# Kernel tuning notes

Measured on AMD Instinct MI355X. Metric: run time of the kernel, lower is better.

Reference implementation:

```python
import jax, jax.numpy as jnp
import numpy as np

N_NODES = 100000
N_EDGES = 1600000
IN_C, HID_C, OUT_C = 128, 64, 32


def setup_inputs() -> dict:
    key = jax.random.key(0)
    k1, k2, k3, k4 = jax.random.split(key, 4)
    x = jax.random.normal(k1, (N_NODES, IN_C), dtype=jnp.float32)
    edge_index = jax.random.randint(k2, (2, N_EDGES), 0, N_NODES, dtype=jnp.int64)
    # glorot-style init for GCN linear weights
    W1 = jax.random.normal(k3, (IN_C, HID_C), dtype=jnp.float32) * (2.0 / (IN_C + HID_C)) ** 0.5
    b1 = jnp.zeros((HID_C,), dtype=jnp.float32)
    W2 = jax.random.normal(k4, (HID_C, OUT_C), dtype=jnp.float32) * (2.0 / (HID_C + OUT_C)) ** 0.5
    b2 = jnp.zeros((OUT_C,), dtype=jnp.float32)
    return {"x": x, "edge_index": edge_index, "W1": W1, "b1": b1, "W2": W2, "b2": b2}


def _gcn_conv(h, row, col, norm, n, b):
    # gather transformed source features, scale by symmetric norm, scatter-add to targets
    msg = h[row] * norm[:, None]            # [E+N, C]
    return jax.ops.segment_sum(msg, col, num_segments=n) + b


def reference(x, edge_index, W1, b1, W2, b2):
    n = x.shape[0]
    loops = jnp.arange(n, dtype=edge_index.dtype)
    row = jnp.concatenate([edge_index[0], loops])   # sources (with self-loops)
    col = jnp.concatenate([edge_index[1], loops])   # targets
    deg = jax.ops.segment_sum(jnp.ones_like(col, dtype=x.dtype), col, num_segments=n)
    dinv = jnp.where(deg > 0, jax.lax.rsqrt(deg), 0.0)
    norm = dinv[row] * dinv[col]                    # D^{-1/2} A_hat D^{-1/2}
    h = jax.nn.relu(_gcn_conv(x @ W1, row, col, norm, n, b1))
    out = _gcn_conv(h @ W2, row, col, norm, n, b2)
    return out
```

## Files before the change

### kernel.cpp

```cpp
#include <hip/hip_runtime.h>

#define IN_C 128
#define HID_C 64
#define OUT_C 32
#define NBLK 512
#define NBUCK 512
#define CAP 5120

__device__ __forceinline__ void f4add(float4& a, const float4 b) {
  a.x += b.x; a.y += b.y; a.z += b.z; a.w += b.w;
}


__global__ void __launch_bounds__(256) scatter_reserve_kernel(
    const int* __restrict__ row, const int* __restrict__ col,
    int* __restrict__ gcur, int* __restrict__ ebuf, int e, int epb) {
  __shared__ int hist[NBUCK];
  __shared__ int cur[NBUCK];
  int t = threadIdx.x, b = blockIdx.x;
  for (int i = t; i < NBUCK; i += 256) hist[i] = 0;
  __syncthreads();
  int s = b * epb, en = min(e, s + epb);
  for (int i = s + t; i < en; i += 256) atomicAdd(&hist[col[i] >> 8], 1);
  __syncthreads();
  for (int i = t; i < NBUCK; i += 256) {
    int h = hist[i];
    int base = h ? atomicAdd(&gcur[i], h) : 0;
    cur[i] = CAP * i + base;
  }
  __syncthreads();
  for (int i = s + t; i < en; i += 256) {
    int c = col[i], r = row[i];
    int bk = c >> 8;
    int p = atomicAdd(&cur[bk], 1);
    if (p < CAP * bk + CAP) ebuf[p] = r | ((c & 255) << 17);
  }
}

__global__ void __launch_bounds__(512) bstart_scan_kernel(const int* __restrict__ gcur,
                                                          int* __restrict__ bstart) {
  __shared__ int s[NBUCK];
  int t = threadIdx.x;
  int v = min(gcur[t], CAP);
  s[t] = v;
  __syncthreads();
  for (int d = 1; d < NBUCK; d <<= 1) {
    int a = (t >= d) ? s[t - d] : 0;
    __syncthreads();
    s[t] += a;
    __syncthreads();
  }
  bstart[t] = s[t] - v;
}

__global__ void __launch_bounds__(256) csr_kernel(const int* __restrict__ ebuf,
                                                  const int* __restrict__ gcur,
                                                  const int* __restrict__ bstart,
                                                  int* __restrict__ offS, int* __restrict__ offE,
                                                  int* __restrict__ srt, float* __restrict__ dinv,
                                                  int n) {
  __shared__ int cnt[256];
  __shared__ int base[256];
  int t = threadIdx.x, b = blockIdx.x;
  int es = b * CAP;
  int ec = min(gcur[b], CAP);
  cnt[t] = 0;
  __syncthreads();
  for (int i = t; i < ec; i += 256) atomicAdd(&cnt[(ebuf[es + i] >> 17) & 255], 1);
  __syncthreads();
  int v = cnt[t];
  base[t] = v;
  __syncthreads();
  for (int d = 1; d < 256; d <<= 1) {
    int a = (t >= d) ? base[t - d] : 0;
    __syncthreads();
    base[t] += a;
    __syncthreads();
  }
  int gstart = bstart[b] + base[t] - v;
  int node = b * 256 + t;
  if (node < n) {
    offS[node] = gstart;
    offE[node] = gstart + v;
    dinv[node] = rsqrtf((float)(v + 1));
  }
  base[t] = gstart;
  __syncthreads();
  for (int i = t; i < ec; i += 256) {
    int pv = ebuf[es + i];
    int pos = atomicAdd(&base[(pv >> 17) & 255], 1);
    srt[pos] = pv & 0x1FFFF;
  }
}


__global__ void gemm1_kernel(const float* __restrict__ x, const float* __restrict__ W1,
                             const float* __restrict__ dinv, float* __restrict__ xw1s, int n) {
  __shared__ float w1s[IN_C * HID_C];
  __shared__ float xs[16 * IN_C];
  int tid = threadIdx.x;
  for (int i = tid; i < IN_C * HID_C; i += 256) w1s[i] = W1[i];
  int row0 = blockIdx.x * 16;
  const float4* x4 = (const float4*)(x + (size_t)row0 * IN_C);
  float4* xs4 = (float4*)xs;
  for (int i = tid; i < 16 * IN_C / 4; i += 256) {
    int grow = row0 + i / (IN_C / 4);
    if (grow < n) xs4[i] = x4[i];
  }
  __syncthreads();
  int r = tid >> 4;
  int c0 = (tid & 15) * 4;
  int row = row0 + r;
  if (row >= n) return;
  float a0 = 0.f, a1 = 0.f, a2 = 0.f, a3 = 0.f;
  const float* xr = xs + r * IN_C;
  for (int k = 0; k < IN_C; ++k) {
    float xv = xr[k];
    const float* w = w1s + k * HID_C + c0;
    a0 += xv * w[0];
    a1 += xv * w[1];
    a2 += xv * w[2];
    a3 += xv * w[3];
  }
  float dv = dinv[row];
  float4 o = {a0 * dv, a1 * dv, a2 * dv, a3 * dv};
  *(float4*)(xw1s + (size_t)row * HID_C + c0) = o;
}

__global__ void __launch_bounds__(256) gather1_gemm2_kernel(
    const int* __restrict__ offS, const int* __restrict__ offE, const int* __restrict__ srt,
    const float* __restrict__ dinv, const float* __restrict__ xw1s,
    const float* __restrict__ b1, const float* __restrict__ W2,
    float* __restrict__ hw2s, int n) {
  __shared__ float w2s[HID_C * OUT_C];
  __shared__ float hs[16][HID_C];
  int t = threadIdx.x;
  for (int i = t; i < HID_C * OUT_C; i += 256) w2s[i] = W2[i];
  int nl = t >> 4;
  int fl = t & 15;
  int c = blockIdx.x * 16 + nl;
  if (c < n) {
    int js = offS[c], je = offE[c];
    float4 a0 = {0.f, 0.f, 0.f, 0.f}, a1 = a0, a2 = a0, a3 = a0;
    int j = js;
    for (; j + 3 < je; j += 4) {
      int r0 = srt[j], r1 = srt[j + 1], r2 = srt[j + 2], r3 = srt[j + 3];
      f4add(a0, ((const float4*)(xw1s + (size_t)r0 * HID_C))[fl]);
      f4add(a1, ((const float4*)(xw1s + (size_t)r1 * HID_C))[fl]);
      f4add(a2, ((const float4*)(xw1s + (size_t)r2 * HID_C))[fl]);
      f4add(a3, ((const float4*)(xw1s + (size_t)r3 * HID_C))[fl]);
    }
    for (; j < je; ++j)
      f4add(a0, ((const float4*)(xw1s + (size_t)srt[j] * HID_C))[fl]);
    f4add(a0, a1); f4add(a2, a3); f4add(a0, a2);
    f4add(a0, ((const float4*)(xw1s + (size_t)c * HID_C))[fl]);
    float dv = dinv[c];
    float4 bb = ((const float4*)b1)[fl];
    float4 hv;
    hv.x = a0.x * dv + bb.x; hv.y = a0.y * dv + bb.y;
    hv.z = a0.z * dv + bb.z; hv.w = a0.w * dv + bb.w;
    hv.x = hv.x > 0.f ? hv.x : 0.f; hv.y = hv.y > 0.f ? hv.y : 0.f;
    hv.z = hv.z > 0.f ? hv.z : 0.f; hv.w = hv.w > 0.f ? hv.w : 0.f;
    ((float4*)hs[nl])[fl] = hv;
  }
  __syncthreads();
  for (int task = t; task < 16 * OUT_C; task += 256) {
    int nl2 = task >> 5, o = task & 31;
    int c2 = blockIdx.x * 16 + nl2;
    if (c2 < n) {
      float a = 0.f;
      const float* hr = hs[nl2];
#pragma unroll
      for (int k = 0; k < HID_C; ++k) a += hr[k] * w2s[k * OUT_C + o];
      hw2s[(size_t)c2 * OUT_C + o] = a * dinv[c2];
    }
  }
}

__global__ void __launch_bounds__(256) gather2_kernel(
    const int* __restrict__ offS, const int* __restrict__ offE, const int* __restrict__ srt,
    const float* __restrict__ dinv, const float* __restrict__ hw2s,
    const float* __restrict__ b2, float* __restrict__ out, int n) {
  int t = threadIdx.x;
  int nl = t >> 3;
  int fl = t & 7;
  int c = blockIdx.x * 32 + nl;
  if (c >= n) return;
  int js = offS[c], je = offE[c];
  float4 a0 = {0.f, 0.f, 0.f, 0.f}, a1 = a0, a2 = a0, a3 = a0;
  int j = js;
  for (; j + 3 < je; j += 4) {
    int r0 = srt[j], r1 = srt[j + 1], r2 = srt[j + 2], r3 = srt[j + 3];
    f4add(a0, ((const float4*)(hw2s + (size_t)r0 * OUT_C))[fl]);
    f4add(a1, ((const float4*)(hw2s + (size_t)r1 * OUT_C))[fl]);
    f4add(a2, ((const float4*)(hw2s + (size_t)r2 * OUT_C))[fl]);
    f4add(a3, ((const float4*)(hw2s + (size_t)r3 * OUT_C))[fl]);
  }
  for (; j < je; ++j)
    f4add(a0, ((const float4*)(hw2s + (size_t)srt[j] * OUT_C))[fl]);
  f4add(a0, a1); f4add(a2, a3); f4add(a0, a2);
  f4add(a0, ((const float4*)(hw2s + (size_t)c * OUT_C))[fl]);
  float dv = dinv[c];
  float4 bb = ((const float4*)b2)[fl];
  float4 o4;
  o4.x = a0.x * dv + bb.x; o4.y = a0.y * dv + bb.y;
  o4.z = a0.z * dv + bb.z; o4.w = a0.w * dv + bb.w;
  ((float4*)(out + (size_t)c * OUT_C))[fl] = o4;
}

extern "C" void kernel_launch(void* const* d_in, const int* in_sizes, int n_in,
                              void* d_out, int out_size, void* d_ws, size_t ws_size,
                              hipStream_t stream) {
  const float* x  = (const float*)d_in[0];
  const int*   ei = (const int*)d_in[1];
  const float* W1 = (const float*)d_in[2];
  const float* b1 = (const float*)d_in[3];
  const float* W2 = (const float*)d_in[4];
  const float* b2 = (const float*)d_in[5];
  float* out = (float*)d_out;

  int n = in_sizes[0] / IN_C;
  int e = in_sizes[1] / 2;
  const int* row = ei;
  const int* col = ei + e;

  float* dinv   = (float*)d_ws;
  int*   offS   = (int*)(dinv + n);
  int*   offE   = offS + n;
  int*   gcur   = offE + n;
  int*   bstart = gcur + NBUCK;
  int*   srt    = bstart + NBUCK;
  float* xw1s   = (float*)(srt + e);
  int*   ebuf   = (int*)xw1s;
  float* hw2s   = xw1s + (size_t)n * HID_C;

  int epb = (e + NBLK - 1) / NBLK;
  int nbuckets = (n + 255) / 256;

  hipMemsetAsync(gcur, 0, NBUCK * sizeof(int), stream);
  hipLaunchKernelGGL(scatter_reserve_kernel, dim3(NBLK), dim3(256), 0, stream,
                     row, col, gcur, ebuf, e, epb);
  hipLaunchKernelGGL(bstart_scan_kernel, dim3(1), dim3(NBUCK), 0, stream, gcur, bstart);
  hipLaunchKernelGGL(csr_kernel, dim3(nbuckets), dim3(256), 0, stream,
                     ebuf, gcur, bstart, offS, offE, srt, dinv, n);
  hipLaunchKernelGGL(gemm1_kernel, dim3((n + 15) / 16), dim3(256), 0, stream,
                     x, W1, dinv, xw1s, n);
  hipLaunchKernelGGL(gather1_gemm2_kernel, dim3((n + 15) / 16), dim3(256), 0, stream,
                     offS, offE, srt, dinv, xw1s, b1, W2, hw2s, n);
  hipLaunchKernelGGL(gather2_kernel, dim3((n + 31) / 32), dim3(256), 0, stream,
                     offS, offE, srt, dinv, hw2s, b2, out, n);
}
```

Measured before the change: 284.0 us.

## Store intermediate features in bf16 and drop bucket-start scan kernel

```diff
diff --git a/kernel.cpp b/kernel.cpp
--- a/kernel.cpp
+++ b/kernel.cpp
@@ -7,8 +7,24 @@
 #define NBUCK 512
 #define CAP 5120
 
-__device__ __forceinline__ void f4add(float4& a, const float4 b) {
-  a.x += b.x; a.y += b.y; a.z += b.z; a.w += b.w;
+typedef unsigned int uint;
+
+__device__ __forceinline__ uint bf16pair(float a, float b) {
+  uint ua = __float_as_uint(a), ub = __float_as_uint(b);
+  ua = (ua + 0x7FFFu + ((ua >> 16) & 1u)) >> 16;
+  ub = (ub + 0x7FFFu + ((ub >> 16) & 1u)) >> 16;
+  return ua | (ub << 16);
+}
+
+__device__ __forceinline__ void acc8(float* acc, uint4 q) {
+  acc[0] += __uint_as_float(q.x << 16);
+  acc[1] += __uint_as_float(q.x & 0xFFFF0000u);
+  acc[2] += __uint_as_float(q.y << 16);
+  acc[3] += __uint_as_float(q.y & 0xFFFF0000u);
+  acc[4] += __uint_as_float(q.z << 16);
+  acc[5] += __uint_as_float(q.z & 0xFFFF0000u);
+  acc[6] += __uint_as_float(q.w << 16);
+  acc[7] += __uint_as_float(q.w & 0xFFFF0000u);
 }
 
 
@@ -37,25 +53,8 @@
   }
 }
 
-__global__ void __launch_bounds__(512) bstart_scan_kernel(const int* __restrict__ gcur,
-                                                          int* __restrict__ bstart) {
-  __shared__ int s[NBUCK];
-  int t = threadIdx.x;
-  int v = min(gcur[t], CAP);
-  s[t] = v;
-  __syncthreads();
-  for (int d = 1; d < NBUCK; d <<= 1) {
-    int a = (t >= d) ? s[t - d] : 0;
-    __syncthreads();
-    s[t] += a;
-    __syncthreads();
-  }
-  bstart[t] = s[t] - v;
-}
-
 __global__ void __launch_bounds__(256) csr_kernel(const int* __restrict__ ebuf,
                                                   const int* __restrict__ gcur,
-                                                  const int* __restrict__ bstart,
                                                   int* __restrict__ offS, int* __restrict__ offE,
                                                   int* __restrict__ srt, float* __restrict__ dinv,
                                                   int n) {
@@ -77,7 +76,7 @@
     base[t] += a;
     __syncthreads();
   }
-  int gstart = bstart[b] + base[t] - v;
+  int gstart = es + base[t] - v;
   int node = b * 256 + t;
   if (node < n) {
     offS[node] = gstart;
@@ -95,7 +94,8 @@
 
 
 __global__ void gemm1_kernel(const float* __restrict__ x, const float* __restrict__ W1,
-                             const float* __restrict__ dinv, float* __restrict__ xw1s, int n) {
+                             const float* __restrict__ dinv, unsigned short* __restrict__ xw1b,
+                             int n) {
   __shared__ float w1s[IN_C * HID_C];
   __shared__ float xs[16 * IN_C];
   int tid = threadIdx.x;
@@ -123,89 +123,116 @@
     a3 += xv * w[3];
   }
   float dv = dinv[row];
-  float4 o = {a0 * dv, a1 * dv, a2 * dv, a3 * dv};
-  *(float4*)(xw1s + (size_t)row * HID_C + c0) = o;
+  uint2 o = make_uint2(bf16pair(a0 * dv, a1 * dv), bf16pair(a2 * dv, a3 * dv));
+  ((uint2*)(xw1b + (size_t)row * HID_C))[tid & 15] = o;
 }
 
 __global__ void __launch_bounds__(256) gather1_gemm2_kernel(
     const int* __restrict__ offS, const int* __restrict__ offE, const int* __restrict__ srt,
-    const float* __restrict__ dinv, const float* __restrict__ xw1s,
+    const float* __restrict__ dinv, const unsigned short* __restrict__ xw1b,
     const float* __restrict__ b1, const float* __restrict__ W2,
-    float* __restrict__ hw2s, int n) {
+    unsigned short* __restrict__ hw2b, int n) {
   __shared__ float w2s[HID_C * OUT_C];
-  __shared__ float hs[16][HID_C];
+  __shared__ float hs[32][HID_C];
   int t = threadIdx.x;
   for (int i = t; i < HID_C * OUT_C; i += 256) w2s[i] = W2[i];
-  int nl = t >> 4;
-  int fl = t & 15;
-  int c = blockIdx.x * 16 + nl;
+  int g = t >> 3, fl = t & 7;
+  int c = blockIdx.x * 32 + g;
   if (c < n) {
     int js = offS[c], je = offE[c];
-    float4 a0 = {0.f, 0.f, 0.f, 0.f}, a1 = a0, a2 = a0, a3 = a0;
+    float acc[8] = {0.f, 0.f, 0.f, 0.f, 0.f, 0.f, 0.f, 0.f};
+    float acc2[8] = {0.f, 0.f, 0.f, 0.f, 0.f, 0.f, 0.f, 0.f};
     int j = js;
     for (; j + 3 < je; j += 4) {
-      int r0 = srt[j], r1 = srt[j + 1], r2 = srt[j + 2], r3 = srt[j + 3];
-      f4add(a0, ((const float4*)(xw1s + (size_t)r0 * HID_C))[fl]);
-      f4add(a1, ((const float4*)(xw1s + (size_t)r1 * HID_C))[fl]);
-      f4add(a2, ((const float4*)(xw1s + (size_t)r2 * HID_C))[fl]);
-      f4add(a3, ((const float4*)(xw1s + (size_t)r3 * HID_C))[fl]);
+      int r0 = __builtin_nontemporal_load(srt + j);
+      int r1 = __builtin_nontemporal_load(srt + j + 1);
+      int r2 = __builtin_nontemporal_load(srt + j + 2);
+      int r3 = __builtin_nontemporal_load(srt + j + 3);
+      uint4 q0 = ((const uint4*)(xw1b + (size_t)r0 * HID_C))[fl];
+      uint4 q1 = ((const uint4*)(xw1b + (size_t)r1 * HID_C))[fl];
+      uint4 q2 = ((const uint4*)(xw1b + (size_t)r2 * HID_C))[fl];
+      uint4 q3 = ((const uint4*)(xw1b + (size_t)r3 * HID_C))[fl];
+      acc8(acc, q0); acc8(acc2, q1); acc8(acc, q2); acc8(acc2, q3);
     }
-    for (; j < je; ++j)
-      f4add(a0, ((const float4*)(xw1s + (size_t)srt[j] * HID_C))[fl]);
-    f4add(a0, a1); f4add(a2, a3); f4add(a0, a2);
-    f4add(a0, ((const float4*)(xw1s + (size_t)c * HID_C))[fl]);
+    for (; j < je; ++j) {
+      int r = __builtin_nontemporal_load(srt + j);
+      acc8(acc, ((const uint4*)(xw1b + (size_t)r * HID_C))[fl]);
+    }
+    acc8(acc, ((const uint4*)(xw1b + (size_t)c * HID_C))[fl]);
     float dv = dinv[c];
-    float4 bb = ((const float4*)b1)[fl];
-    float4 hv;
-    hv.x = a0.x * dv + bb.x; hv.y = a0.y * dv + bb.y;
-    hv.z = a0.z * dv + bb.z; hv.w = a0.w * dv + bb.w;
-    hv.x = hv.x > 0.f ? hv.x : 0.f; hv.y = hv.y > 0.f ? hv.y : 0.f;
-    hv.z = hv.z > 0.f ? hv.z : 0.f; hv.w = hv.w > 0.f ? hv.w : 0.f;
-    ((float4*)hs[nl])[fl] = hv;
-  }
-  __syncthreads();
-  for (int task = t; task < 16 * OUT_C; task += 256) {
-    int nl2 = task >> 5, o = task & 31;
-    int c2 = blockIdx.x * 16 + nl2;
+    const float4* b1v = (const float4*)b1;
+    float4 blo = b1v[fl * 2], bhi = b1v[fl * 2 + 1];
+    float h0 = (acc[0] + acc2[0]) * dv + blo.x;
+    float h1 = (acc[1] + acc2[1]) * dv + blo.y;
+    float h2 = (acc[2] + acc2[2]) * dv + blo.z;
+    float h3 = (acc[3] + acc2[3]) * dv + blo.w;
+    float h4 = (acc[4] + acc2[4]) * dv + bhi.x;
+    float h5 = (acc[5] + acc2[5]) * dv + bhi.y;
+    float h6 = (acc[6] + acc2[6]) * dv + bhi.z;
+    float h7 = (acc[7] + acc2[7]) * dv + bhi.w;
+    float4 lo = {h0 > 0.f ? h0 : 0.f, h1 > 0.f ? h1 : 0.f,
+                 h2 > 0.f ? h2 : 0.f, h3 > 0.f ? h3 : 0.f};
+    float4 hi = {h4 > 0.f ? h4 : 0.f, h5 > 0.f ? h5 : 0.f,
+                 h6 > 0.f ? h6 : 0.f, h7 > 0.f ? h7 : 0.f};
+    ((float4*)hs[g])[fl * 2] = lo;
+    ((float4*)hs[g])[fl * 2 + 1] = hi;
+  }
+  __syncthreads();
+  for (int task = t; task < 32 * (OUT_C / 2); task += 256) {
+    int nl = task >> 4, pr = task & 15;
+    int c2 = blockIdx.x * 32 + nl;
     if (c2 < n) {
-      float a = 0.f;
-      const float* hr = hs[nl2];
+      float s0 = 0.f, s1 = 0.f;
+      const float* hr = hs[nl];
 #pragma unroll
-      for (int k = 0; k < HID_C; ++k) a += hr[k] * w2s[k * OUT_C + o];
-      hw2s[(size_t)c2 * OUT_C + o] = a * dinv[c2];
+      for (int k = 0; k < HID_C; ++k) {
+        float hv = hr[k];
+        s0 += hv * w2s[k * OUT_C + pr * 2];
+        s1 += hv * w2s[k * OUT_C + pr * 2 + 1];
+      }
+      float dv2 = dinv[c2];
+      ((uint*)(hw2b + (size_t)c2 * OUT_C))[pr] = bf16pair(s0 * dv2, s1 * dv2);
     }
   }
 }
 
 __global__ void __launch_bounds__(256) gather2_kernel(
     const int* __restrict__ offS, const int* __restrict__ offE, const int* __restrict__ srt,
-    const float* __restrict__ dinv, const float* __restrict__ hw2s,
+    const float* __restrict__ dinv, const unsigned short* __restrict__ hw2b,
     const float* __restrict__ b2, float* __restrict__ out, int n) {
   int t = threadIdx.x;
-  int nl = t >> 3;
-  int fl = t & 7;
-  int c = blockIdx.x * 32 + nl;
+  int g = t >> 2, fl = t & 3;
+  int c = blockIdx.x * 64 + g;
   if (c >= n) return;
   int js = offS[c], je = offE[c];
-  float4 a0 = {0.f, 0.f, 0.f, 0.f}, a1 = a0, a2 = a0, a3 = a0;
+  float acc[8] = {0.f, 0.f, 0.f, 0.f, 0.f, 0.f, 0.f, 0.f};
+  float acc2[8] = {0.f, 0.f, 0.f, 0.f, 0.f, 0.f, 0.f, 0.f};
   int j = js;
   for (; j + 3 < je; j += 4) {
-    int r0 = srt[j], r1 = srt[j + 1], r2 = srt[j + 2], r3 = srt[j + 3];
-    f4add(a0, ((const float4*)(hw2s + (size_t)r0 * OUT_C))[fl]);
-    f4add(a1, ((const float4*)(hw2s + (size_t)r1 * OUT_C))[fl]);
-    f4add(a2, ((const float4*)(hw2s + (size_t)r2 * OUT_C))[fl]);
-    f4add(a3, ((const float4*)(hw2s + (size_t)r3 * OUT_C))[fl]);
-  }
-  for (; j < je; ++j)
-    f4add(a0, ((const float4*)(hw2s + (size_t)srt[j] * OUT_C))[fl]);
-  f4add(a0, a1); f4add(a2, a3); f4add(a0, a2);
-  f4add(a0, ((const float4*)(hw2s + (size_t)c * OUT_C))[fl]);
+    int r0 = __builtin_nontemporal_load(srt + j);
+    int r1 = __builtin_nontemporal_load(srt + j + 1);
+    int r2 = __builtin_nontemporal_load(srt + j + 2);
+    int r3 = __builtin_nontemporal_load(srt + j + 3);
+    uint4 q0 = ((const uint4*)(hw2b + (size_t)r0 * OUT_C))[fl];
+    uint4 q1 = ((const uint4*)(hw2b + (size_t)r1 * OUT_C))[fl];
+    uint4 q2 = ((const uint4*)(hw2b + (size_t)r2 * OUT_C))[fl];
+    uint4 q3 = ((const uint4*)(hw2b + (size_t)r3 * OUT_C))[fl];
+    acc8(acc, q0); acc8(acc2, q1); acc8(acc, q2); acc8(acc2, q3);
+  }
+  for (; j < je; ++j) {
+    int r = __builtin_nontemporal_load(srt + j);
+    acc8(acc, ((const uint4*)(hw2b + (size_t)r * OUT_C))[fl]);
+  }
+  acc8(acc, ((const uint4*)(hw2b + (size_t)c * OUT_C))[fl]);
   float dv = dinv[c];
-  float4 bb = ((const float4*)b2)[fl];
-  float4 o4;
-  o4.x = a0.x * dv + bb.x; o4.y = a0.y * dv + bb.y;
-  o4.z = a0.z * dv + bb.z; o4.w = a0.w * dv + bb.w;
-  ((float4*)(out + (size_t)c * OUT_C))[fl] = o4;
+  const float4* b2v = (const float4*)b2;
+  float4 blo = b2v[fl * 2], bhi = b2v[fl * 2 + 1];
+  float4 olo = {(acc[0] + acc2[0]) * dv + blo.x, (acc[1] + acc2[1]) * dv + blo.y,
+                (acc[2] + acc2[2]) * dv + blo.z, (acc[3] + acc2[3]) * dv + blo.w};
+  float4 ohi = {(acc[4] + acc2[4]) * dv + bhi.x, (acc[5] + acc2[5]) * dv + bhi.y,
+                (acc[6] + acc2[6]) * dv + bhi.z, (acc[7] + acc2[7]) * dv + bhi.w};
+  ((float4*)(out + (size_t)c * OUT_C))[fl * 2] = olo;
+  ((float4*)(out + (size_t)c * OUT_C))[fl * 2 + 1] = ohi;
 }
 
 extern "C" void kernel_launch(void* const* d_in, const int* in_sizes, int n_in,
@@ -224,15 +251,14 @@
   const int* row = ei;
   const int* col = ei + e;
 
-  float* dinv   = (float*)d_ws;
-  int*   offS   = (int*)(dinv + n);
-  int*   offE   = offS + n;
-  int*   gcur   = offE + n;
-  int*   bstart = gcur + NBUCK;
-  int*   srt    = bstart + NBUCK;
-  float* xw1s   = (float*)(srt + e);
-  int*   ebuf   = (int*)xw1s;
-  float* hw2s   = xw1s + (size_t)n * HID_C;
+  float* dinv = (float*)d_ws;
+  int*   offS = (int*)(dinv + n);
+  int*   offE = offS + n;
+  int*   gcur = offE + n;
+  int*   srt  = gcur + NBUCK;
+  unsigned short* xw1b = (unsigned short*)(srt + (size_t)NBUCK * CAP);
+  int*   ebuf = (int*)xw1b;
+  unsigned short* hw2b = xw1b + (size_t)n * HID_C;
 
   int epb = (e + NBLK - 1) / NBLK;
   int nbuckets = (n + 255) / 256;
@@ -240,13 +266,12 @@
   hipMemsetAsync(gcur, 0, NBUCK * sizeof(int), stream);
   hipLaunchKernelGGL(scatter_reserve_kernel, dim3(NBLK), dim3(256), 0, stream,
                      row, col, gcur, ebuf, e, epb);
-  hipLaunchKernelGGL(bstart_scan_kernel, dim3(1), dim3(NBUCK), 0, stream, gcur, bstart);
   hipLaunchKernelGGL(csr_kernel, dim3(nbuckets), dim3(256), 0, stream,
-                     ebuf, gcur, bstart, offS, offE, srt, dinv, n);
+                     ebuf, gcur, offS, offE, srt, dinv, n);
   hipLaunchKernelGGL(gemm1_kernel, dim3((n + 15) / 16), dim3(256), 0, stream,
-                     x, W1, dinv, xw1s, n);
-  hipLaunchKernelGGL(gather1_gemm2_kernel, dim3((n + 15) / 16), dim3(256), 0, stream,
-                     offS, offE, srt, dinv, xw1s, b1, W2, hw2s, n);
-  hipLaunchKernelGGL(gather2_kernel, dim3((n + 31) / 32), dim3(256), 0, stream,
-                     offS, offE, srt, dinv, hw2s, b2, out, n);
-}
+                     x, W1, dinv, xw1b, n);
+  hipLaunchKernelGGL(gather1_gemm2_kernel, dim3((n + 31) / 32), dim3(256), 0, stream,
+                     offS, offE, srt, dinv, xw1b, b1, W2, hw2b, n);
+  hipLaunchKernelGGL(gather2_kernel, dim3((n + 63) / 64), dim3(256), 0, stream,
+                     offS, offE, srt, dinv, hw2b, b2, out, n);
+}
```

Result: faster. 253.7 us (-10.7%).
